# Optimization experiments

Measured on AMD Instinct MI355X. Metric: run time of the kernel, lower is better.

The kernel has to match this reference:

```python
import jax, jax.numpy as jnp
import numpy as np

N_NODES = 50000
N_EDGES = 200000
IN_DIM = 512
HID = 2000
LAT = 128


def setup_inputs() -> dict:
    key = jax.random.key(0)
    ks = jax.random.split(key, 6)
    x = jax.random.normal(ks[0], (N_NODES, IN_DIM), dtype=jnp.float32)
    edge_index = jax.random.randint(ks[1], (2, N_EDGES), 0, N_NODES, dtype=jnp.int64)
    # glorot-ish scales so ReLU/Sigmoid stay in a sane range
    W1 = jax.random.normal(ks[2], (IN_DIM, HID), dtype=jnp.float32) * (1.0 / np.sqrt(IN_DIM))
    b1 = jnp.zeros((HID,), dtype=jnp.float32)
    W2 = jax.random.normal(ks[3], (HID, LAT), dtype=jnp.float32) * (1.0 / np.sqrt(HID))
    b2 = jnp.zeros((LAT,), dtype=jnp.float32)
    return {"x": x, "edge_index": edge_index, "W1": W1, "b1": b1, "W2": W2, "b2": b2}


def gcn_conv(x, edge_index, W, b):
    """PyG GCNConv: D^-1/2 (A+I) D^-1/2 (X W) + b, unit edge weights."""
    n = x.shape[0]
    loops = jnp.arange(n, dtype=edge_index.dtype)
    row = jnp.concatenate([edge_index[0], loops])  # source nodes
    col = jnp.concatenate([edge_index[1], loops])  # target nodes
    deg = jax.ops.segment_sum(jnp.ones_like(col, dtype=x.dtype), col, num_segments=n)
    dis = jnp.where(deg > 0, jax.lax.rsqrt(deg), 0.0)  # deg^-1/2, inf -> 0
    norm = dis[row] * dis[col]                         # [E+N]
    h = x @ W                                          # transform first: [N, out]
    msg = h[row] * norm[:, None]                       # gather + normalize: [E+N, out]
    out = jax.ops.segment_sum(msg, col, num_segments=n)  # scatter-add
    return out + b


def reference(x, edge_index, W1, b1, W2, b2):
    h = jax.nn.relu(gcn_conv(x, edge_index, W1, b1))
    return jax.nn.sigmoid(gcn_conv(h, edge_index, W2, b2))
```

## Files before the change

kernel.cpp:

```cpp
#include <hip/hip_runtime.h>
#include <hip/hip_fp16.h>

#define NN 50000
#define NE 200000
#define IND 512
#define HIDD 2000
#define LATD 128

#define M_PAD 50048
#define N1_PAD 2048
#define MT1 391
#define SLAB1 49
#define NBLK 196

typedef _Float16 f16x8 __attribute__((ext_vector_type(8)));
typedef float f32x4 __attribute__((ext_vector_type(4)));

__device__ __forceinline__ void gload_lds16(const _Float16* g, _Float16* l) {
    __builtin_amdgcn_global_load_lds(
        (const __attribute__((address_space(1))) unsigned int*)g,
        (__attribute__((address_space(3))) unsigned int*)l,
        16, 0, 0);
}

__global__ void k_degree(const int* __restrict__ col, int* __restrict__ deg) {
    int e = blockIdx.x * 256 + threadIdx.x;
    if (e < NE) atomicAdd(&deg[col[e]], 1);
}

__global__ void k_dis(const int* __restrict__ deg, float* __restrict__ dis) {
    int i = blockIdx.x * 256 + threadIdx.x;
    if (i < NN) dis[i] = rsqrtf((float)deg[i] + 1.0f);
}

__global__ void k_bsum(const int* __restrict__ deg, int* __restrict__ bsum) {
    __shared__ int sm[4];
    int i = blockIdx.x * 256 + threadIdx.x;
    int v = (i < NN) ? deg[i] : 0;
    #pragma unroll
    for (int off = 32; off; off >>= 1) v += __shfl_down(v, off, 64);
    if ((threadIdx.x & 63) == 0) sm[threadIdx.x >> 6] = v;
    __syncthreads();
    if (threadIdx.x == 0) bsum[blockIdx.x] = sm[0] + sm[1] + sm[2] + sm[3];
}

__global__ void k_bscan(int* __restrict__ bsum) {
    __shared__ int sm[256];
    int tid = threadIdx.x;
    int v = (tid < NBLK) ? bsum[tid] : 0;
    sm[tid] = v;
    __syncthreads();
    #pragma unroll
    for (int off = 1; off < 256; off <<= 1) {
        int t = (tid >= off) ? sm[tid - off] : 0;
        __syncthreads();
        sm[tid] += t;
        __syncthreads();
    }
    if (tid < NBLK) bsum[tid] = sm[tid] - v;
}

__global__ void k_scan_final(const int* __restrict__ deg, const int* __restrict__ bsum,
                             int* __restrict__ row_ptr) {
    __shared__ int sm[256];
    int b = blockIdx.x, tid = threadIdx.x;
    int i = b * 256 + tid;
    int v = (i < NN) ? deg[i] : 0;
    sm[tid] = v;
    __syncthreads();
    #pragma unroll
    for (int off = 1; off < 256; off <<= 1) {
        int t = (tid >= off) ? sm[tid - off] : 0;
        __syncthreads();
        sm[tid] += t;
        __syncthreads();
    }
    if (i < NN) row_ptr[i] = bsum[b] + sm[tid] - v;
    if (i == NN - 1) row_ptr[NN] = bsum[b] + sm[tid];
}

__global__ void k_fill(const int* __restrict__ ei, const int* __restrict__ row_ptr,
                       int* __restrict__ cursor, int* __restrict__ csr_src) {
    int e = blockIdx.x * 256 + threadIdx.x;
    if (e < NE) {
        int r = ei[e], c = ei[NE + e];
        int pos = atomicAdd(&cursor[c], 1);
        csr_src[row_ptr[c] + pos] = r;
    }
}

__global__ void k_transpose_tiled(const float* __restrict__ in,
                                  _Float16* __restrict__ out, int R, int C, int ldo) {
    __shared__ float sm[32][33];
    int c0 = blockIdx.x * 32, r0 = blockIdx.y * 32;
    int tx = threadIdx.x & 31, ty = threadIdx.x >> 5;
    #pragma unroll
    for (int i = 0; i < 4; ++i) {
        int r = r0 + ty + i * 8, c = c0 + tx;
        sm[ty + i * 8][tx] = (r < R && c < C) ? in[(size_t)r * C + c] : 0.f;
    }
    __syncthreads();
    #pragma unroll
    for (int i = 0; i < 4; ++i) {
        int c = c0 + ty + i * 8, r = r0 + tx;
        if (c < C && r < R) out[(size_t)c * ldo + r] = (_Float16)sm[tx][ty + i * 8];
    }
}

__global__ void k_xcvt(const float* __restrict__ in, _Float16* __restrict__ out, int n8) {
    int i = blockIdx.x * 256 + threadIdx.x;
    if (i < n8) {
        float4 a = ((const float4*)in)[i * 2];
        float4 b = ((const float4*)in)[i * 2 + 1];
        f16x8 o;
        o[0] = (_Float16)a.x; o[1] = (_Float16)a.y; o[2] = (_Float16)a.z; o[3] = (_Float16)a.w;
        o[4] = (_Float16)b.x; o[5] = (_Float16)b.y; o[6] = (_Float16)b.z; o[7] = (_Float16)b.w;
        ((f16x8*)out)[i] = o;
    }
}

__global__ void k_gather_x(const _Float16* __restrict__ xh, const int* __restrict__ row_ptr,
                           const int* __restrict__ csr_src, const float* __restrict__ dis,
                           _Float16* __restrict__ Ah) {
    int dst = blockIdx.x * 4 + (threadIdx.x >> 6);
    if (dst >= NN) return;
    int lane = threadIdx.x & 63;
    float dd = dis[dst];
    f16x8 sv = *(const f16x8*)(xh + (size_t)dst * IND + lane * 8);
    float acc[8];
    #pragma unroll
    for (int i = 0; i < 8; ++i) acc[i] = dd * (float)sv[i];
    int beg = row_ptr[dst], end = row_ptr[dst + 1];
    for (int i = beg; i < end; ++i) {
        int s = csr_src[i];
        float ns = dis[s];
        f16x8 v = *(const f16x8*)(xh + (size_t)s * IND + lane * 8);
        #pragma unroll
        for (int q = 0; q < 8; ++q) acc[q] += ns * (float)v[q];
    }
    f16x8 o;
    #pragma unroll
    for (int i = 0; i < 8; ++i) o[i] = (_Float16)(dd * acc[i]);
    *(f16x8*)(Ah + (size_t)dst * IND + lane * 8) = o;
}

__global__ void k_gather_t(const float* __restrict__ t, const int* __restrict__ row_ptr,
                           const int* __restrict__ csr_src, const float* __restrict__ dis,
                           const float* __restrict__ b2, float* __restrict__ out) {
    int dst = blockIdx.x * 4 + (threadIdx.x >> 6);
    if (dst >= NN) return;
    int lane = threadIdx.x & 63;
    float dd = dis[dst];
    float2 td = *(const float2*)(t + (size_t)dst * LATD + lane * 2);
    float accx = dd * td.x, accy = dd * td.y;
    int beg = row_ptr[dst], end = row_ptr[dst + 1];
    for (int i = beg; i < end; ++i) {
        int s = csr_src[i];
        float ns = dis[s];
        float2 ts = *(const float2*)(t + (size_t)s * LATD + lane * 2);
        accx += ns * ts.x; accy += ns * ts.y;
    }
    float2 bb = *(const float2*)(b2 + lane * 2);
    float vx = dd * accx + bb.x;
    float vy = dd * accy + bb.y;
    float2 o;
    o.x = 1.0f / (1.0f + __expf(-vx));
    o.y = 1.0f / (1.0f + __expf(-vy));
    *(float2*)(out + (size_t)dst * LATD + lane * 2) = o;
}

__global__ __launch_bounds__(256, 2) void k_gemm1(
    const _Float16* __restrict__ A,
    const _Float16* __restrict__ Bt,
    const float* __restrict__ bias,
    _Float16* __restrict__ Ch)
{
    const int b = blockIdx.x;
    const int mT = (b & 7) * SLAB1 + ((b >> 3) >> 4);
    const int nT = (b >> 3) & 15;
    if (mT >= MT1) return;
    const int mBase = mT * 128;
    const int nBase = nT * 128;

    __shared__ __align__(16) _Float16 As[2 * 128 * 32];
    __shared__ __align__(16) _Float16 Bs[2 * 128 * 32];

    const int tid = threadIdx.x;
    const int lane = tid & 63;
    const int w = tid >> 6;

    const int srow = w * 32 + (lane >> 2);
    const int scol = (lane & 3) * 8;
    const _Float16* Ag0 = A + (size_t)(mBase + srow) * IND + scol;
    const _Float16* Ag1 = Ag0 + (size_t)16 * IND;
    const _Float16* Bg0 = Bt + (size_t)(nBase + srow) * IND + scol;
    const _Float16* Bg1 = Bg0 + (size_t)16 * IND;

    const int wm = (w >> 1) * 64;
    const int wn = (w & 1) * 64;
    const int lm = lane & 15;
    const int quad = lane >> 4;

    f32x4 acc[4][4];
    #pragma unroll
    for (int i = 0; i < 4; ++i)
        #pragma unroll
        for (int j = 0; j < 4; ++j)
            acc[i][j] = (f32x4){0.f, 0.f, 0.f, 0.f};

    for (int k0 = 0; k0 < IND; k0 += 64) {
        #pragma unroll
        for (int s = 0; s < 2; ++s) {
            gload_lds16(Ag0 + k0 + s * 32, As + s * 4096 + w * 1024);
            gload_lds16(Ag1 + k0 + s * 32, As + s * 4096 + w * 1024 + 512);
            gload_lds16(Bg0 + k0 + s * 32, Bs + s * 4096 + w * 1024);
            gload_lds16(Bg1 + k0 + s * 32, Bs + s * 4096 + w * 1024 + 512);
        }
        __syncthreads();

        #pragma unroll
        for (int s = 0; s < 2; ++s) {
            f16x8 af[4], bfr[4];
            #pragma unroll
            for (int mi = 0; mi < 4; ++mi)
                af[mi] = *(const f16x8*)&As[s * 4096 + (wm + mi * 16 + lm) * 32 + quad * 8];
            #pragma unroll
            for (int ni = 0; ni < 4; ++ni)
                bfr[ni] = *(const f16x8*)&Bs[s * 4096 + (wn + ni * 16 + lm) * 32 + quad * 8];
            #pragma unroll
            for (int mi = 0; mi < 4; ++mi)
                #pragma unroll
                for (int ni = 0; ni < 4; ++ni)
                    acc[mi][ni] = __builtin_amdgcn_mfma_f32_16x16x32_f16(
                        af[mi], bfr[ni], acc[mi][ni], 0, 0, 0);
        }
        __syncthreads();
    }

    #pragma unroll
    for (int mi = 0; mi < 4; ++mi) {
        #pragma unroll
        for (int ni = 0; ni < 4; ++ni) {
            int col = nBase + wn + ni * 16 + lm;
            float bval = bias[col];
            #pragma unroll
            for (int r = 0; r < 4; ++r) {
                int rowg = mBase + wm + mi * 16 + quad * 4 + r;
                float v = fmaxf(acc[mi][ni][r] + bval, 0.f);
                Ch[(size_t)rowg * N1_PAD + col] = (_Float16)v;
            }
        }
    }
}

__global__ __launch_bounds__(256, 2) void k_gemm2(
    const _Float16* __restrict__ A,
    const _Float16* __restrict__ Bt,
    float* __restrict__ Cf)
{
    __shared__ __align__(16) _Float16 As[2 * 64 * 32];
    __shared__ __align__(16) _Float16 Bs[2 * 128 * 32];

    const int tid = threadIdx.x;
    const int lane = tid & 63;
    const int w = tid >> 6;
    const int mBase = blockIdx.x * 64;

    const int srA = w * 16 + (lane >> 2);
    const int srB = w * 32 + (lane >> 2);
    const int scol = (lane & 3) * 8;
    const _Float16* Ag  = A + (size_t)(mBase + srA) * N1_PAD + scol;
    const _Float16* Bg0 = Bt + (size_t)srB * N1_PAD + scol;
    const _Float16* Bg1 = Bg0 + (size_t)16 * N1_PAD;

    const int wm = (w & 1) * 32;
    const int wn = (w >> 1) * 64;
    const int lm = lane & 15;
    const int quad = lane >> 4;

    f32x4 acc[2][4];
    #pragma unroll
    for (int i = 0; i < 2; ++i)
        #pragma unroll
        for (int j = 0; j < 4; ++j)
            acc[i][j] = (f32x4){0.f, 0.f, 0.f, 0.f};

    for (int k0 = 0; k0 < N1_PAD; k0 += 64) {
        #pragma unroll
        for (int s = 0; s < 2; ++s) {
            gload_lds16(Ag + k0 + s * 32, As + s * 2048 + w * 512);
            gload_lds16(Bg0 + k0 + s * 32, Bs + s * 4096 + w * 1024);
            gload_lds16(Bg1 + k0 + s * 32, Bs + s * 4096 + w * 1024 + 512);
        }
        __syncthreads();

        #pragma unroll
        for (int s = 0; s < 2; ++s) {
            f16x8 af[2], bfr[4];
            #pragma unroll
            for (int mi = 0; mi < 2; ++mi)
                af[mi] = *(const f16x8*)&As[s * 2048 + (wm + mi * 16 + lm) * 32 + quad * 8];
            #pragma unroll
            for (int ni = 0; ni < 4; ++ni)
                bfr[ni] = *(const f16x8*)&Bs[s * 4096 + (wn + ni * 16 + lm) * 32 + quad * 8];
            #pragma unroll
            for (int mi = 0; mi < 2; ++mi)
                #pragma unroll
                for (int ni = 0; ni < 4; ++ni)
                    acc[mi][ni] = __builtin_amdgcn_mfma_f32_16x16x32_f16(
                        af[mi], bfr[ni], acc[mi][ni], 0, 0, 0);
        }
        __syncthreads();
    }

    #pragma unroll
    for (int mi = 0; mi < 2; ++mi) {
        #pragma unroll
        for (int ni = 0; ni < 4; ++ni) {
            int col = wn + ni * 16 + lm;
            #pragma unroll
            for (int r = 0; r < 4; ++r) {
                int rowg = mBase + wm + mi * 16 + quad * 4 + r;
                Cf[(size_t)rowg * LATD + col] = acc[mi][ni][r];
            }
        }
    }
}

extern "C" void kernel_launch(void* const* d_in, const int* in_sizes, int n_in,
                              void* d_out, int out_size, void* d_ws, size_t ws_size,
                              hipStream_t stream) {
    const float* x  = (const float*)d_in[0];
    const int* ei   = (const int*)d_in[1];
    const float* W1 = (const float*)d_in[2];
    const float* b1 = (const float*)d_in[3];
    const float* W2 = (const float*)d_in[4];
    const float* b2 = (const float*)d_in[5];
    float* out = (float*)d_out;

    char* p = (char*)d_ws;
    auto alloc = [&](size_t bytes) {
        char* q = p; p += (bytes + 255) & ~(size_t)255; return q;
    };
    int* deg        = (int*)alloc((size_t)NN * 4);
    int* bsum       = (int*)alloc((size_t)NBLK * 4);
    int* row_ptr    = (int*)alloc((size_t)(NN + 1) * 4);
    int* cursor     = (int*)alloc((size_t)NN * 4);
    int* csr_src    = (int*)alloc((size_t)NE * 4);
    float* dis      = (float*)alloc((size_t)NN * 4);
    float* b1pad    = (float*)alloc((size_t)N1_PAD * 4);
    _Float16* W1T   = (_Float16*)alloc((size_t)N1_PAD * IND * 2);
    _Float16* W2T   = (_Float16*)alloc((size_t)LATD * N1_PAD * 2);
    _Float16* xh    = (_Float16*)alloc((size_t)NN * IND * 2);
    _Float16* Ah    = (_Float16*)alloc((size_t)M_PAD * IND * 2);
    _Float16* h     = (_Float16*)alloc((size_t)M_PAD * N1_PAD * 2);
    float* t        = (float*)alloc((size_t)M_PAD * LATD * 4);

    hipMemsetAsync(deg,    0, (size_t)NN * 4, stream);
    hipMemsetAsync(cursor, 0, (size_t)NN * 4, stream);
    hipMemsetAsync(b1pad,  0, (size_t)N1_PAD * 4, stream);
    hipMemsetAsync(W1T,    0, (size_t)N1_PAD * IND * 2, stream);
    hipMemsetAsync(W2T,    0, (size_t)LATD * N1_PAD * 2, stream);
    hipMemcpyAsync(b1pad, b1, (size_t)HIDD * 4, hipMemcpyDeviceToDevice, stream);

    k_degree<<<(NE + 255) / 256, 256, 0, stream>>>(ei + NE, deg);
    k_dis<<<(NN + 255) / 256, 256, 0, stream>>>(deg, dis);
    k_bsum<<<NBLK, 256, 0, stream>>>(deg, bsum);
    k_bscan<<<1, 256, 0, stream>>>(bsum);
    k_scan_final<<<NBLK, 256, 0, stream>>>(deg, bsum, row_ptr);
    k_fill<<<(NE + 255) / 256, 256, 0, stream>>>(ei, row_ptr, cursor, csr_src);

    {
        dim3 gt1((HIDD + 31) / 32, (IND + 31) / 32);
        k_transpose_tiled<<<gt1, 256, 0, stream>>>(W1, W1T, IND, HIDD, IND);
        dim3 gt2((LATD + 31) / 32, (HIDD + 31) / 32);
        k_transpose_tiled<<<gt2, 256, 0, stream>>>(W2, W2T, HIDD, LATD, N1_PAD);
        k_xcvt<<<(NN * IND / 8 + 255) / 256, 256, 0, stream>>>(x, xh, NN * IND / 8);
    }

    k_gather_x<<<(NN + 3) / 4, 256, 0, stream>>>(xh, row_ptr, csr_src, dis, Ah);

    k_gemm1<<<8 * SLAB1 * 16, 256, 0, stream>>>(Ah, W1T, b1pad, h);
    k_gemm2<<<M_PAD / 64, 256, 0, stream>>>(h, W2T, t);

    k_gather_t<<<(NN + 3) / 4, 256, 0, stream>>>(t, row_ptr, csr_src, dis, b2, out);
}
```

Before: 505.9 us.

## Rewrite GEMM1 as 256x256 tile, 8-wave, ping-pong pipelined kernel with swizzled LDS

Replaces the 128x128, 4-wave GEMM1 with a 256x256 tile computed by 8 waves. The K loop is double-buffered and interleaves global-to-LDS loads of later k-slices with MFMA work on the current slice, using explicit barriers, vmcnt waits and setprio. LDS rows are XOR-swizzled to avoid bank conflicts, and the M padding grows to a multiple of 256. The aim is more data reuse per tile and hiding of memory latency behind the MFMAs, at the cost of 128KB LDS per block, fewer blocks, more padded rows, and fragile hand-written synchronisation.

```diff
diff --git a/kernel.cpp b/kernel.cpp
--- a/kernel.cpp
+++ b/kernel.cpp
@@ -7,10 +7,8 @@
 #define HIDD 2000
 #define LATD 128
 
-#define M_PAD 50048
+#define M_PAD 50176
 #define N1_PAD 2048
-#define MT1 391
-#define SLAB1 49
 #define NBLK 196
 
 typedef _Float16 f16x8 __attribute__((ext_vector_type(8)));
@@ -169,85 +167,164 @@
     *(float2*)(out + (size_t)dst * LATD + lane * 2) = o;
 }
 
-__global__ __launch_bounds__(256, 2) void k_gemm1(
+
+#define AOFFB(buf, h) ((buf) * 65536 + (h) * 16384)
+#define BOFFB(buf, h) ((buf) * 65536 + 32768 + (h) * 16384)
+
+__device__ __forceinline__ void g1_bar() {
+    asm volatile("" ::: "memory");
+    __builtin_amdgcn_s_barrier();
+    asm volatile("" ::: "memory");
+}
+
+__device__ __forceinline__ void stage_ht(const _Float16* __restrict__ g, int grow0, int kt,
+                                         _Float16* smem, int region_byte, int tid) {
+    const int w = tid >> 6;
+    const int r = tid >> 3;
+    const int sw = ((tid & 7) * 16) ^ ((r & 7) << 4);
+    const _Float16* s0 = g + (size_t)(grow0 + r) * IND + kt * 64 + (sw >> 1);
+    _Float16* d = smem + (region_byte >> 1) + w * 512;
+    gload_lds16(s0, d);
+    gload_lds16(s0 + (size_t)64 * IND, d + 4096);
+}
+
+#define G1_RD(off) (*(const f16x8*)(sb + (off)))
+#define G1_RDA(buf, h) { _Pragma("unroll") for (int mi_ = 0; mi_ < 4; ++mi_) { \
+    int rb_ = AOFFB(buf, h) + (ra + mi_ * 16) * 128; \
+    a[mi_][0] = G1_RD(rb_ + ck0); a[mi_][1] = G1_RD(rb_ + ck1); } }
+#define G1_RDB(buf, h, P) { _Pragma("unroll") for (int ni_ = 0; ni_ < 2; ++ni_) { \
+    int rb_ = BOFFB(buf, h) + (rbb + ni_ * 16) * 128; \
+    bfr[P][ni_][0] = G1_RD(rb_ + ck0); bfr[P][ni_][1] = G1_RD(rb_ + ck1); } }
+#define G1_MFMA(Q, P) { __builtin_amdgcn_s_setprio(1); \
+    _Pragma("unroll") for (int ks_ = 0; ks_ < 2; ++ks_) \
+    _Pragma("unroll") for (int mi_ = 0; mi_ < 4; ++mi_) \
+    _Pragma("unroll") for (int ni_ = 0; ni_ < 2; ++ni_) \
+        acc[Q][P][mi_][ni_] = __builtin_amdgcn_mfma_f32_16x16x32_f16( \
+            a[mi_][ks_], bfr[P][ni_][ks_], acc[Q][P][mi_][ni_], 0, 0, 0); \
+    __builtin_amdgcn_s_setprio(0); }
+
+template<bool LAST>
+__device__ __forceinline__ void g1_iter(const _Float16* __restrict__ A,
+                                        const _Float16* __restrict__ Bt,
+                                        _Float16* smem, const char* sb,
+                                        int t, int mBase, int nBase, int tid,
+                                        int ra, int rbb, int ck0, int ck1,
+                                        f32x4 (&acc)[2][2][4][2]) {
+    f16x8 a[4][2], bfr[2][2][2];
+    G1_RDA(0, 0); G1_RDB(0, 0, 0);
+    stage_ht(Bt, nBase + 128, t + 1, smem, BOFFB(1, 1), tid);
+    g1_bar();
+    G1_MFMA(0, 0);
+    g1_bar();
+    G1_RDB(0, 1, 1);
+    if (!LAST) stage_ht(A, mBase, t + 2, smem, AOFFB(0, 0), tid);
+    g1_bar();
+    G1_MFMA(0, 1);
+    g1_bar();
+    G1_RDA(0, 1);
+    if (!LAST) stage_ht(Bt, nBase, t + 2, smem, BOFFB(0, 0), tid);
+    g1_bar();
+    G1_MFMA(1, 0);
+    g1_bar();
+    if (!LAST) stage_ht(A, mBase + 128, t + 2, smem, AOFFB(0, 1), tid);
+    g1_bar();
+    G1_MFMA(1, 1);
+    if (LAST) { asm volatile("s_waitcnt vmcnt(0)" ::: "memory"); }
+    else      { asm volatile("s_waitcnt vmcnt(6)" ::: "memory"); }
+    g1_bar();
+    G1_RDA(1, 0); G1_RDB(1, 0, 0);
+    if (!LAST) stage_ht(Bt, nBase + 128, t + 2, smem, BOFFB(0, 1), tid);
+    g1_bar();
+    G1_MFMA(0, 0);
+    g1_bar();
+    G1_RDB(1, 1, 1);
+    if (!LAST) stage_ht(A, mBase, t + 3, smem, AOFFB(1, 0), tid);
+    g1_bar();
+    G1_MFMA(0, 1);
+    g1_bar();
+    G1_RDA(1, 1);
+    if (!LAST) stage_ht(Bt, nBase, t + 3, smem, BOFFB(1, 0), tid);
+    g1_bar();
+    G1_MFMA(1, 0);
+    g1_bar();
+    if (!LAST) stage_ht(A, mBase + 128, t + 3, smem, AOFFB(1, 1), tid);
+    g1_bar();
+    G1_MFMA(1, 1);
+    if (!LAST) {
+        asm volatile("s_waitcnt vmcnt(6)" ::: "memory");
+        g1_bar();
+    }
+}
+
+__global__ __launch_bounds__(512, 2) void k_gemm1(
     const _Float16* __restrict__ A,
     const _Float16* __restrict__ Bt,
     const float* __restrict__ bias,
     _Float16* __restrict__ Ch)
 {
-    const int b = blockIdx.x;
-    const int mT = (b & 7) * SLAB1 + ((b >> 3) >> 4);
-    const int nT = (b >> 3) & 15;
-    if (mT >= MT1) return;
-    const int mBase = mT * 128;
-    const int nBase = nT * 128;
-
-    __shared__ __align__(16) _Float16 As[2 * 128 * 32];
-    __shared__ __align__(16) _Float16 Bs[2 * 128 * 32];
+    __shared__ __align__(16) _Float16 smem[65536];
+
+    const int b0 = blockIdx.x;
+    const int swz = (b0 & 7) * 196 + (b0 >> 3);
+    const int mT = swz >> 3, nT = swz & 7;
+    const int mBase = mT * 256, nBase = nT * 256;
 
     const int tid = threadIdx.x;
     const int lane = tid & 63;
     const int w = tid >> 6;
-
-    const int srow = w * 32 + (lane >> 2);
-    const int scol = (lane & 3) * 8;
-    const _Float16* Ag0 = A + (size_t)(mBase + srow) * IND + scol;
-    const _Float16* Ag1 = Ag0 + (size_t)16 * IND;
-    const _Float16* Bg0 = Bt + (size_t)(nBase + srow) * IND + scol;
-    const _Float16* Bg1 = Bg0 + (size_t)16 * IND;
-
-    const int wm = (w >> 1) * 64;
-    const int wn = (w & 1) * 64;
-    const int lm = lane & 15;
-    const int quad = lane >> 4;
-
-    f32x4 acc[4][4];
-    #pragma unroll
-    for (int i = 0; i < 4; ++i)
-        #pragma unroll
-        for (int j = 0; j < 4; ++j)
-            acc[i][j] = (f32x4){0.f, 0.f, 0.f, 0.f};
-
-    for (int k0 = 0; k0 < IND; k0 += 64) {
-        #pragma unroll
-        for (int s = 0; s < 2; ++s) {
-            gload_lds16(Ag0 + k0 + s * 32, As + s * 4096 + w * 1024);
-            gload_lds16(Ag1 + k0 + s * 32, As + s * 4096 + w * 1024 + 512);
-            gload_lds16(Bg0 + k0 + s * 32, Bs + s * 4096 + w * 1024);
-            gload_lds16(Bg1 + k0 + s * 32, Bs + s * 4096 + w * 1024 + 512);
-        }
-        __syncthreads();
-
-        #pragma unroll
-        for (int s = 0; s < 2; ++s) {
-            f16x8 af[4], bfr[4];
-            #pragma unroll
-            for (int mi = 0; mi < 4; ++mi)
-                af[mi] = *(const f16x8*)&As[s * 4096 + (wm + mi * 16 + lm) * 32 + quad * 8];
-            #pragma unroll
-            for (int ni = 0; ni < 4; ++ni)
-                bfr[ni] = *(const f16x8*)&Bs[s * 4096 + (wn + ni * 16 + lm) * 32 + quad * 8];
+    const int wr = w >> 2, wc = w & 3;
+    const int lm = lane & 15, quad = lane >> 4;
+    const int ra  = wr * 64 + lm;
+    const int rbb = wc * 32 + lm;
+    const int x7  = (lm & 7) << 4;
+    const int ck0 = (quad * 16) ^ x7;
+    const int ck1 = (64 + quad * 16) ^ x7;
+    const char* sb = (const char*)smem;
+
+    f32x4 acc[2][2][4][2];
+    #pragma unroll
+    for (int q = 0; q < 2; ++q)
+        #pragma unroll
+        for (int p = 0; p < 2; ++p)
             #pragma unroll
             for (int mi = 0; mi < 4; ++mi)
                 #pragma unroll
-                for (int ni = 0; ni < 4; ++ni)
-                    acc[mi][ni] = __builtin_amdgcn_mfma_f32_16x16x32_f16(
-                        af[mi], bfr[ni], acc[mi][ni], 0, 0, 0);
-        }
-        __syncthreads();
-    }
-
-    #pragma unroll
-    for (int mi = 0; mi < 4; ++mi) {
-        #pragma unroll
-        for (int ni = 0; ni < 4; ++ni) {
-            int col = nBase + wn + ni * 16 + lm;
-            float bval = bias[col];
-            #pragma unroll
-            for (int r = 0; r < 4; ++r) {
-                int rowg = mBase + wm + mi * 16 + quad * 4 + r;
-                float v = fmaxf(acc[mi][ni][r] + bval, 0.f);
-                Ch[(size_t)rowg * N1_PAD + col] = (_Float16)v;
+                for (int ni = 0; ni < 2; ++ni)
+                    acc[q][p][mi][ni] = (f32x4){0.f, 0.f, 0.f, 0.f};
+
+    stage_ht(A,  mBase,       0, smem, AOFFB(0, 0), tid);
+    stage_ht(Bt, nBase,       0, smem, BOFFB(0, 0), tid);
+    stage_ht(A,  mBase + 128, 0, smem, AOFFB(0, 1), tid);
+    stage_ht(Bt, nBase + 128, 0, smem, BOFFB(0, 1), tid);
+    stage_ht(A,  mBase,       1, smem, AOFFB(1, 0), tid);
+    stage_ht(Bt, nBase,       1, smem, BOFFB(1, 0), tid);
+    stage_ht(A,  mBase + 128, 1, smem, AOFFB(1, 1), tid);
+    asm volatile("s_waitcnt vmcnt(6)" ::: "memory");
+    g1_bar();
+
+    #pragma unroll 1
+    for (int it = 0; it < IND / 128 - 1; ++it)
+        g1_iter<false>(A, Bt, smem, sb, 2 * it, mBase, nBase, tid, ra, rbb, ck0, ck1, acc);
+    g1_iter<true>(A, Bt, smem, sb, IND / 64 - 2, mBase, nBase, tid, ra, rbb, ck0, ck1, acc);
+
+    #pragma unroll
+    for (int q = 0; q < 2; ++q) {
+        #pragma unroll
+        for (int p = 0; p < 2; ++p) {
+            #pragma unroll
+            for (int ni = 0; ni < 2; ++ni) {
+                int col = nBase + p * 128 + wc * 32 + ni * 16 + lm;
+                float bv = bias[col];
+                #pragma unroll
+                for (int mi = 0; mi < 4; ++mi) {
+                    int rowg = mBase + q * 128 + wr * 64 + mi * 16 + quad * 4;
+                    f32x4 v = acc[q][p][mi][ni];
+                    #pragma unroll
+                    for (int r = 0; r < 4; ++r) {
+                        float x = fmaxf(v[r] + bv, 0.f);
+                        Ch[(size_t)(rowg + r) * N1_PAD + col] = (_Float16)x;
+                    }
+                }
             }
         }
     }
@@ -380,7 +457,7 @@
 
     k_gather_x<<<(NN + 3) / 4, 256, 0, stream>>>(xh, row_ptr, csr_src, dis, Ah);
 
-    k_gemm1<<<8 * SLAB1 * 16, 256, 0, stream>>>(Ah, W1T, b1pad, h);
+    k_gemm1<<<(M_PAD / 256) * (N1_PAD / 256), 512, 0, stream>>>(Ah, W1T, b1pad, h);
     k_gemm2<<<M_PAD / 64, 256, 0, stream>>>(h, W2T, t);
 
     k_gather_t<<<(NN + 3) / 4, 256, 0, stream>>>(t, row_ptr, csr_src, dis, b2, out);
```

New measurement: 522.9 us. 3.4% more time.
